# Kernel optimization log

Hardware: AMD Instinct MI355X
Metric: run time of the kernel (lower is better)

## Reference

```python
import jax, jax.numpy as jnp
import numpy as np

B, S, H = 8, 160, 128
W_SIZE, V_SIZE, A_SIZE = 300, 35, 74


def setup_inputs() -> dict:
    key = jax.random.key(0)
    keys = iter(jax.random.split(key, 80))

    def rn(shape, scale=0.05):
        return jax.random.normal(next(keys), shape, dtype=jnp.float32) * scale

    inp = {}
    inp["w"] = rn((B, S, W_SIZE), 1.0)
    inp["v"] = rn((B, S, V_SIZE), 1.0)
    inp["a"] = rn((B, S, A_SIZE), 1.0)
    inp["lengths"] = jnp.full((B,), S, dtype=jnp.int32)  # full-length sequences

    def add_lstm(p, in_size, h_size):
        inp[p + "_Wih"] = rn((4 * h_size, in_size))
        inp[p + "_Whh"] = rn((4 * h_size, h_size))
        inp[p + "_bih"] = rn((4 * h_size,))
        inp[p + "_bhh"] = rn((4 * h_size,))

    add_lstm("w", W_SIZE, H)
    add_lstm("v", V_SIZE, H)
    add_lstm("a", A_SIZE, H)
    add_lstm("c", 3 * H, 3 * H)

    def add_xattn(p, h):
        inp[p + "_W1"] = rn((h, 2 * h))  # Linear(2h, h)
        inp[p + "_b1"] = rn((h,))
        inp[p + "_w2"] = rn((h,))        # Linear(h, 1, bias=False)

    add_xattn("vw", H)
    add_xattn("aw", H)
    add_xattn("sa", 3 * H)

    inp["mp_w"] = rn((H,))
    inp["mp_b"] = rn((1,))
    inp["fc1_W"] = rn((H, 5 * H))
    inp["fc1_b"] = rn((H,))
    inp["fc2_W"] = rn((1, H))
    inp["fc2_b"] = rn((1,))
    return inp


def lstm(x, Wih, Whh, bih, bhh):
    # single-layer batch_first LSTM, PyTorch gate order (i, f, g, o)
    b = x.shape[0]
    h = Whh.shape[1]
    xg = jnp.einsum('bsi,gi->bsg', x, Wih) + bih + bhh  # [B,S,4H]

    def step(carry, xt):
        hp, cp = carry
        g = xt + hp @ Whh.T
        i, f, gg, o = jnp.split(g, 4, axis=-1)
        c = jax.nn.sigmoid(f) * cp + jax.nn.sigmoid(i) * jnp.tanh(gg)
        hn = jax.nn.sigmoid(o) * jnp.tanh(c)
        return (hn, c), hn

    init = (jnp.zeros((b, h), x.dtype), jnp.zeros((b, h), x.dtype))
    _, hs = jax.lax.scan(step, init, jnp.swapaxes(xg, 0, 1))
    return jnp.swapaxes(hs, 0, 1)  # [B,S,H]


def cross_attention(src_hs, tgt_hs, mask, W1, b1, w2):
    # additive (Bahdanau) attention; attn_1(cat([src, tgt])) split into two GEMMs
    h = src_hs.shape[-1]
    s = src_hs @ W1[:, :h].T              # [B,V,Hd]
    t = tgt_hs @ W1[:, h:].T + b1         # [B,W,Hd]
    # [B,W,V,Hd] broadcast-add + tanh, then reduce with w2 -> scores [B,W,V]
    scores = jnp.einsum('bwvd,d->bwv', jnp.tanh(t[:, :, None, :] + s[:, None, :, :]), w2)
    scores = mask * scores                # multiplicative mask (as in original)
    weights = jax.nn.softmax(scores, axis=2)
    out = jnp.einsum('bwv,bvh->bwh', weights, src_hs)
    return out, weights


def soft_attention(reps, w, b):
    weights = jax.nn.softmax(reps @ w + b[0], axis=1)  # [B,S]
    out = jnp.einsum('bs,bsh->bh', weights, reps)
    return out, weights[:, :, None]


def reference(w, v, a, lengths,
              w_Wih, w_Whh, w_bih, w_bhh,
              v_Wih, v_Whh, v_bih, v_bhh,
              a_Wih, a_Whh, a_bih, a_bhh,
              c_Wih, c_Whh, c_bih, c_bhh,
              vw_W1, vw_b1, vw_w2,
              aw_W1, aw_b1, aw_w2,
              sa_W1, sa_b1, sa_w2,
              mp_w, mp_b, fc1_W, fc1_b, fc2_W, fc2_b):
    b, s = w.shape[0], w.shape[1]
    w_hs = lstm(w, w_Wih, w_Whh, w_bih, w_bhh)
    v_hs = lstm(v, v_Wih, v_Whh, v_bih, v_bhh)
    a_hs = lstm(a, a_Wih, a_Whh, a_bih, a_bhh)

    len_mask = (jnp.arange(s)[None, :] < lengths[:, None]).astype(w_hs.dtype)  # [B,S]
    mask3 = jnp.broadcast_to(len_mask[:, None, :], (b, s, s))                  # [B,W,V]

    v_out, v_attn_w = cross_attention(v_hs, w_hs, mask3, vw_W1, vw_b1, vw_w2)
    a_out, a_attn_w = cross_attention(a_hs, w_hs, mask3, aw_W1, aw_b1, aw_w2)

    c_hs = lstm(jnp.concatenate([w_hs, v_out, a_out], axis=2), c_Wih, c_Whh, c_bih, c_bhh)
    c_attn_out, _ = cross_attention(c_hs, c_hs, mask3, sa_W1, sa_b1, sa_w2)
    c_out = c_attn_out[jnp.arange(b), lengths - 1]  # last valid timestep, [B,3H]

    v_comp, v_soft_w = soft_attention(v_hs, mp_w, mp_b)
    a_comp, a_soft_w = soft_attention(a_hs, mp_w, mp_b)

    feat = jnp.concatenate([c_out, v_comp, a_comp], axis=-1)  # [B,5H]
    out = jax.nn.relu(feat @ fc1_W.T + fc1_b) @ fc2_W.T + fc2_b  # dropout = identity (eval)
    return out.reshape(-1), v_attn_w, v_soft_w, a_attn_w, a_soft_w
```

## Files before the change

### kernel.cpp

```cpp
#include <hip/hip_runtime.h>
#include <hip/hip_fp16.h>

typedef unsigned int u32;
typedef unsigned long long u64;

#define B 8
#define S 160
#define H 128
#define H3 384
#define G4 512
#define CG 1536
#define WIN 300
#define VIN 35
#define AIN 74

#define XG_W   0
#define XG_V   (XG_W + B*S*G4)
#define XG_A   (XG_V + B*S*G4)
#define HS_W   (XG_A + B*S*G4)
#define HS_V   (HS_W + B*S*H)
#define HS_A   (HS_V + B*S*H)
#define S_VW   (HS_A + B*S*H)
#define T_VW   (S_VW + B*S*H)
#define S_AW   (T_VW + B*S*H)
#define T_AW   (S_AW + B*S*H)
#define C_X    (T_AW + B*S*H)
#define S_SA   (C_X + B*S*H3)
#define WIHT_W (S_SA + B*S*H3)
#define WIHT_V (WIHT_W + WIN*G4)
#define WIHT_A (WIHT_V + VIN*G4)
#define WIHT_C (WIHT_A + AIN*G4)
#define WHHT_W (WIHT_C + H3*CG)
#define WHHT_V (WHHT_W + H*G4)
#define WHHT_A (WHHT_V + H*G4)
#define SAT_S  (WHHT_A + H*G4)
#define SAT_T  (SAT_S + H3*H3)
#define VW_ST  (SAT_T + H3*H3)
#define VW_TT  (VW_ST + H*H)
#define AW_ST  (VW_TT + H*H)
#define AW_TT  (AW_ST + H*H)
#define BSUM_W (AW_TT + H*H)
#define BSUM_V (BSUM_W + G4)
#define BSUM_A (BSUM_V + G4)
#define BSUM_C (BSUM_A + G4)
#define VCOMP  (BSUM_C + CG)
#define ACOMP  (VCOMP + B*H)
#define C_OUT  (ACOMP + B*H)
#define XGC16  (C_OUT + B*H3)
#define WRES   (XGC16 + B*S*CG/2)
#define CHS16  (WRES + CG*H3/2)
#define H_X    (CHS16 + B*S*H3/2)

#define O_VATT  8
#define O_VSOFT (8 + B*S*S)
#define O_AATT  (O_VSOFT + B*S)
#define O_ASOFT (O_AATT + B*S*S)

#define REP32(M) M(0)M(1)M(2)M(3)M(4)M(5)M(6)M(7)M(8)M(9)M(10)M(11)M(12)M(13)M(14)M(15)M(16)M(17)M(18)M(19)M(20)M(21)M(22)M(23)M(24)M(25)M(26)M(27)M(28)M(29)M(30)M(31)
#define REP48(M) REP32(M) M(32)M(33)M(34)M(35)M(36)M(37)M(38)M(39)M(40)M(41)M(42)M(43)M(44)M(45)M(46)M(47)

__device__ __forceinline__ float sigf(float x){ return 1.f/(1.f+__expf(-x)); }
__device__ __forceinline__ float tanhfast(float x){ float e=__expf(2.f*x); return 1.f - 2.f/(e+1.f); }
__device__ __forceinline__ float wred_sum(float x){
#pragma unroll
  for (int o=32;o;o>>=1) x += __shfl_xor(x,o);
  return x;
}
__device__ __forceinline__ float wred_max(float x){
#pragma unroll
  for (int o=32;o;o>>=1) x = fmaxf(x,__shfl_xor(x,o));
  return x;
}
__device__ __forceinline__ u32 packh2(float lo, float hi){
  __half a=__float2half_rn(lo), b=__float2half_rn(hi);
  return ((u32)__half_as_ushort(b)<<16) | (u32)__half_as_ushort(a);
}

typedef _Float16 h2v __attribute__((ext_vector_type(2)));
#if defined(__has_builtin)
#if __has_builtin(__builtin_amdgcn_fdot2)
#define HAVE_FDOT2 1
#endif
#endif
__device__ __forceinline__ float fdot2f(u32 w, u32 h, float acc){
#ifdef HAVE_FDOT2
  return __builtin_amdgcn_fdot2(__builtin_bit_cast(h2v,w), __builtin_bit_cast(h2v,h), acc, false);
#else
  h2v a=__builtin_bit_cast(h2v,w), b=__builtin_bit_cast(h2v,h);
  return acc + (float)a.x*(float)b.x + (float)a.y*(float)b.y;
#endif
}

#define PREP_TOT (3*G4 + CG + WIN*G4 + VIN*G4 + AIN*G4 + H3*CG + 3*H*G4 + 2*H3*H3 + 4*H*H + CG*H3/2)
__global__ void k0_prep(float* __restrict__ ws, u32* __restrict__ wsu,
    const float* __restrict__ wWih, const float* __restrict__ wWhh, const float* __restrict__ wbih, const float* __restrict__ wbhh,
    const float* __restrict__ vWih, const float* __restrict__ vWhh, const float* __restrict__ vbih, const float* __restrict__ vbhh,
    const float* __restrict__ aWih, const float* __restrict__ aWhh, const float* __restrict__ abih, const float* __restrict__ abhh,
    const float* __restrict__ cWih, const float* __restrict__ cWhh, const float* __restrict__ cbih, const float* __restrict__ cbhh,
    const float* __restrict__ vwW1, const float* __restrict__ awW1, const float* __restrict__ saW1)
{
  int idx = blockIdx.x*256 + threadIdx.x;
  if (idx >= PREP_TOT) return;
  if (idx < G4){ ws[BSUM_W+idx]=wbih[idx]+wbhh[idx]; return; } idx -= G4;
  if (idx < G4){ ws[BSUM_V+idx]=vbih[idx]+vbhh[idx]; return; } idx -= G4;
  if (idx < G4){ ws[BSUM_A+idx]=abih[idx]+abhh[idx]; return; } idx -= G4;
  if (idx < CG){ ws[BSUM_C+idx]=cbih[idx]+cbhh[idx]; return; } idx -= CG;
  if (idx < WIN*G4){ int k=idx/G4,g=idx%G4; ws[WIHT_W+idx]=wWih[g*WIN+k]; return; } idx -= WIN*G4;
  if (idx < VIN*G4){ int k=idx/G4,g=idx%G4; ws[WIHT_V+idx]=vWih[g*VIN+k]; return; } idx -= VIN*G4;
  if (idx < AIN*G4){ int k=idx/G4,g=idx%G4; ws[WIHT_A+idx]=aWih[g*AIN+k]; return; } idx -= AIN*G4;
  if (idx < H3*CG){ int k=idx/CG,g=idx%CG; ws[WIHT_C+idx]=cWih[g*H3+k]; return; } idx -= H3*CG;
  if (idx < H*G4){ int q=idx&3, r=idx>>2, g=r&511, k4=r>>9; ws[WHHT_W+idx]=wWhh[g*H + 4*k4+q]; return; } idx -= H*G4;
  if (idx < H*G4){ int q=idx&3, r=idx>>2, g=r&511, k4=r>>9; ws[WHHT_V+idx]=vWhh[g*H + 4*k4+q]; return; } idx -= H*G4;
  if (idx < H*G4){ int q=idx&3, r=idx>>2, g=r&511, k4=r>>9; ws[WHHT_A+idx]=aWhh[g*H + 4*k4+q]; return; } idx -= H*G4;
  if (idx < H3*H3){ int k=idx/H3,d=idx%H3; ws[SAT_S+idx]=saW1[d*(2*H3)+k]; return; } idx -= H3*H3;
  if (idx < H3*H3){ int k=idx/H3,d=idx%H3; ws[SAT_T+idx]=saW1[d*(2*H3)+H3+k]; return; } idx -= H3*H3;
  if (idx < H*H){ int k=idx/H,d=idx%H; ws[VW_ST+idx]=vwW1[d*(2*H)+k]; return; } idx -= H*H;
  if (idx < H*H){ int k=idx/H,d=idx%H; ws[VW_TT+idx]=vwW1[d*(2*H)+H+k]; return; } idx -= H*H;
  if (idx < H*H){ int k=idx/H,d=idx%H; ws[AW_ST+idx]=awW1[d*(2*H)+k]; return; } idx -= H*H;
  if (idx < H*H){ int k=idx/H,d=idx%H; ws[AW_TT+idx]=awW1[d*(2*H)+H+k]; return; } idx -= H*H;
  {
    int q = idx & 3; int r = idx >> 2;
    int t = r & 255; int r2 = r >> 8;
    int i = r2 % 48; int sl = r2 / 48;
    int j = t >> 6, ul = t & 63;
    int row = j*H3 + sl*64 + ul;
    int k2 = i*4 + q;
    wsu[WRES+idx] = packh2(cWhh[(size_t)row*H3 + 2*k2], cWhh[(size_t)row*H3 + 2*k2 + 1]);
  }
}

__global__ void k1_xg(float* __restrict__ ws,
    const float* __restrict__ xw, const float* __restrict__ xv, const float* __restrict__ xa)
{
  int bid = blockIdx.x;
  int lstm = bid/160; int rem = bid%160; int b = rem/20; int s0 = (rem%20)*8;
  int in_dim; const float* x; const float* wT; const float* bs; float* xg;
  if (lstm==0){ in_dim=WIN; x=xw; wT=ws+WIHT_W; bs=ws+BSUM_W; xg=ws+XG_W; }
  else if (lstm==1){ in_dim=VIN; x=xv; wT=ws+WIHT_V; bs=ws+BSUM_V; xg=ws+XG_V; }
  else { in_dim=AIN; x=xa; wT=ws+WIHT_A; bs=ws+BSUM_A; xg=ws+XG_A; }
  __shared__ float xt[8][WIN];
  int tid = threadIdx.x;
  for (int i=tid; i<8*in_dim; i+=256){ int r=i/in_dim, k=i%in_dim; xt[r][k] = x[((size_t)(b*S+s0+r))*in_dim + k]; }
  __syncthreads();
  float acc0[8], acc1[8];
  float b0 = bs[tid], b1 = bs[tid+256];
#pragma unroll
  for (int r=0;r<8;r++){ acc0[r]=b0; acc1[r]=b1; }
  for (int k=0;k<in_dim;k++){
    float w0 = wT[k*G4 + tid], w1 = wT[k*G4 + 256 + tid];
#pragma unroll
    for (int r=0;r<8;r++){ float xx = xt[r][k]; acc0[r] = fmaf(xx,w0,acc0[r]); acc1[r] = fmaf(xx,w1,acc1[r]); }
  }
#pragma unroll
  for (int r=0;r<8;r++){
    size_t ro = (size_t)(b*S+s0+r)*G4;
    xg[ro + tid] = acc0[r];
    xg[ro + 256 + tid] = acc1[r];
  }
}

__global__ __launch_bounds__(512,1) void k2_lstm(float* __restrict__ ws)
{
  int lstm = blockIdx.x >> 3, b = blockIdx.x & 7;
  const float* xg; const float* whhT; float* hs; float* cx = nullptr;
  if (lstm==0){ xg=ws+XG_W; whhT=ws+WHHT_W; hs=ws+HS_W; cx=ws+C_X; }
  else if (lstm==1){ xg=ws+XG_V; whhT=ws+WHHT_V; hs=ws+HS_V; }
  else { xg=ws+XG_A; whhT=ws+WHHT_A; hs=ws+HS_A; }
  int g = threadIdx.x;
  const float4* wb = ((const float4*)whhT) + g;
#define K2_LD(i) float4 w##i = wb[(i)*512];
  REP32(K2_LD)
  __shared__ __align__(16) float hbuf[H];
  __shared__ float gsum[G4];
  float c_reg = 0.f;
  if (g < H) hbuf[g] = 0.f;
  const float* xgb = xg + (size_t)b*S*G4;
  float* hsb = hs + (size_t)b*S*H;
  float* cxb = cx ? cx + (size_t)b*S*H3 : nullptr;
  float xg_cur = xgb[g];
  __syncthreads();
  const float4* h4p = (const float4*)hbuf;
  for (int t=0;t<S;t++){
    float acc = xg_cur;
    float xg_nxt = (t+1<S) ? xgb[(size_t)(t+1)*G4 + g] : 0.f;
#define K2_FMA(i) { float4 h4 = h4p[i]; acc = fmaf(w##i.x,h4.x,acc); acc = fmaf(w##i.y,h4.y,acc); acc = fmaf(w##i.z,h4.z,acc); acc = fmaf(w##i.w,h4.w,acc); }
    REP32(K2_FMA)
    gsum[g] = acc;
    xg_cur = xg_nxt;
    __syncthreads();
    if (g < H){
      float gi=gsum[g], gf=gsum[H+g], gg=gsum[2*H+g], go=gsum[3*H+g];
      c_reg = sigf(gf)*c_reg + sigf(gi)*tanhfast(gg);
      float h = sigf(go)*tanhfast(c_reg);
      hbuf[g] = h;
      hsb[(size_t)t*H + g] = h;
      if (cxb) cxb[(size_t)t*H3 + g] = h;
    }
    __syncthreads();
  }
}

__global__ void k3a_proj(float* __restrict__ ws, const float* __restrict__ vwb1, const float* __restrict__ awb1)
{
  int bid = blockIdx.x;
  int p = bid/160; int rem = bid%160; int b = rem/20; int s0 = (rem%20)*8;
  const float* src; const float* wT; const float* bias=nullptr; float* dst;
  if (p==0){ src=ws+HS_V; wT=ws+VW_ST; dst=ws+S_VW; }
  else if (p==1){ src=ws+HS_W; wT=ws+VW_TT; bias=vwb1; dst=ws+T_VW; }
  else if (p==2){ src=ws+HS_A; wT=ws+AW_ST; dst=ws+S_AW; }
  else { src=ws+HS_W; wT=ws+AW_TT; bias=awb1; dst=ws+T_AW; }
  __shared__ float xr[8][H];
  int tid = threadIdx.x;
  for (int i=tid;i<8*H;i+=128){ int r=i>>7, k=i&127; xr[r][k] = src[(size_t)(b*S+s0+r)*H + k]; }
  __syncthreads();
  float acc[8];
  float bv = bias ? bias[tid] : 0.f;
#pragma unroll
  for (int r=0;r<8;r++) acc[r]=bv;
  for (int k=0;k<H;k++){
    float wv = wT[k*H + tid];
#pragma unroll
    for (int r=0;r<8;r++) acc[r] = fmaf(xr[r][k], wv, acc[r]);
  }
#pragma unroll
  for (int r=0;r<8;r++) dst[(size_t)(b*S+s0+r)*H + tid] = acc[r];
}

__global__ void k3b_attn(float* __restrict__ ws, float* __restrict__ dout,
    const int* __restrict__ lengths, const float* __restrict__ vww2, const float* __restrict__ aww2)
{
  int wid = threadIdx.x >> 6, lane = threadIdx.x & 63;
  int row = blockIdx.x*4 + wid;
  int A = row / (B*S); int rem = row % (B*S); int b = rem / S; int w = rem % S;
  const float* sp = ws + (A? S_AW : S_VW) + (size_t)(b*S)*H;
  const float* tp = ws + (A? T_AW : T_VW) + (size_t)(b*S + w)*H;
  const float* w2 = A? aww2 : vww2;
  const float* src = ws + (A? HS_A : HS_V) + (size_t)(b*S)*H;
  float* attw = dout + (A? O_AATT : O_VATT) + (size_t)b*S*S + (size_t)w*S;
  int len = lengths[b];
  __shared__ float sc[4][S];
  float2 t2 = ((const float2*)tp)[lane];
  float2 w22 = ((const float2*)w2)[lane];
  for (int v=0; v<S; v++){
    float2 s2 = ((const float2*)(sp + (size_t)v*H))[lane];
    float x0 = tanhfast(t2.x + s2.x), x1 = tanhfast(t2.y + s2.y);
    float p = wred_sum(x0*w22.x + x1*w22.y);
    if (lane==0) sc[wid][v] = p;
  }
  __syncthreads();
  float m0 = (lane      < len)? sc[wid][lane]     : 0.f;
  float m1 = (lane+64   < len)? sc[wid][lane+64]  : 0.f;
  float m2 = (lane<32) ? ((lane+128 < len)? sc[wid][lane+128] : 0.f) : -1e30f;
  float m = wred_max(fmaxf(fmaxf(m0,m1),m2));
  float e0 = __expf(m0-m), e1 = __expf(m1-m), e2 = (lane<32)? __expf(m2-m) : 0.f;
  float inv = 1.f / wred_sum(e0+e1+e2);
  e0*=inv; e1*=inv; e2*=inv;
  sc[wid][lane] = e0; sc[wid][lane+64] = e1; if (lane<32) sc[wid][128+lane] = e2;
  attw[lane] = e0; attw[lane+64] = e1; if (lane<32) attw[128+lane] = e2;
  __syncthreads();
  float2 acc; acc.x=0.f; acc.y=0.f;
  for (int v=0; v<S; v++){
    float wg = sc[wid][v];
    float2 sv = ((const float2*)(src + (size_t)v*H))[lane];
    acc.x = fmaf(wg, sv.x, acc.x); acc.y = fmaf(wg, sv.y, acc.y);
  }
  float* cxr = ws + C_X + (size_t)(b*S + w)*H3 + (A? 2*H : H);
  ((float2*)cxr)[lane] = acc;
}

__global__ void k4_soft(float* __restrict__ ws, float* __restrict__ dout,
    const float* __restrict__ mpw, const float* __restrict__ mpb)
{
  int A = blockIdx.x >> 3, b = blockIdx.x & 7;
  const float* reps = ws + (A? HS_A : HS_V) + (size_t)(b*S)*H;
  float* softw = dout + (A? O_ASOFT : O_VSOFT) + b*S;
  float* comp = ws + (A? ACOMP : VCOMP) + b*H;
  __shared__ float sc[S]; __shared__ float wg[S];
  int wid = threadIdx.x >> 6, lane = threadIdx.x & 63;
  float bb = mpb[0];
  for (int s=wid; s<S; s+=4){
    float2 r2 = ((const float2*)(reps + (size_t)s*H))[lane];
    float2 m2 = ((const float2*)mpw)[lane];
    float p = wred_sum(r2.x*m2.x + r2.y*m2.y);
    if (lane==0) sc[s] = p + bb;
  }
  __syncthreads();
  if (threadIdx.x < 64){
    float m0 = sc[lane], m1 = sc[lane+64], m2 = (lane<32)? sc[lane+128] : -1e30f;
    float m = wred_max(fmaxf(fmaxf(m0,m1),m2));
    float e0=__expf(m0-m), e1=__expf(m1-m), e2=(lane<32)?__expf(m2-m):0.f;
    float inv = 1.f / wred_sum(e0+e1+e2);
    e0*=inv; e1*=inv; e2*=inv;
    wg[lane]=e0; wg[lane+64]=e1; if (lane<32) wg[128+lane]=e2;
    softw[lane]=e0; softw[lane+64]=e1; if (lane<32) softw[128+lane]=e2;
  }
  __syncthreads();
  if (threadIdx.x < H){
    float acc=0.f;
    for (int s=0;s<S;s++) acc = fmaf(wg[s], reps[(size_t)s*H + threadIdx.x], acc);
    comp[threadIdx.x] = acc;
  }
}

__global__ void k5_xgc(float* __restrict__ ws, u32* __restrict__ wsu)
{
  int b = blockIdx.x/40; int s0 = (blockIdx.x%40)*4;
  const float* cxb = ws + C_X + (size_t)(b*S+s0)*H3;
  const float* wT = ws + WIHT_C;
  const float* bs = ws + BSUM_C;
  __half* xgc = (__half*)(wsu + XGC16);
  __shared__ float xr[4][H3];
  int tid = threadIdx.x;
  for (int i=tid;i<4*H3;i+=512){ int r=i/H3, k=i%H3; xr[r][k]=cxb[(size_t)r*H3+k]; }
  __syncthreads();
  float acc[4][3];
  float b0=bs[tid], b1=bs[tid+512], b2=bs[tid+1024];
#pragma unroll
  for (int r=0;r<4;r++){ acc[r][0]=b0; acc[r][1]=b1; acc[r][2]=b2; }
  for (int k=0;k<H3;k++){
    float w0=wT[(size_t)k*CG+tid], w1=wT[(size_t)k*CG+512+tid], w2v=wT[(size_t)k*CG+1024+tid];
#pragma unroll
    for (int r=0;r<4;r++){
      float xx = xr[r][k];
      acc[r][0]=fmaf(xx,w0,acc[r][0]); acc[r][1]=fmaf(xx,w1,acc[r][1]); acc[r][2]=fmaf(xx,w2v,acc[r][2]);
    }
  }
#pragma unroll
  for (int r=0;r<4;r++){
    size_t ro = (size_t)(b*S + s0+r)*CG;
    xgc[ro + tid]        = __float2half_rn(acc[r][0]);
    xgc[ro + 512 + tid]  = __float2half_rn(acc[r][1]);
    xgc[ro + 1024 + tid] = __float2half_rn(acc[r][2]);
  }
}

__global__ __launch_bounds__(256,1) void k6_clstm(float* __restrict__ ws, u32* __restrict__ wsu)
{
  int b = blockIdx.x & 7, sl = blockIdx.x >> 3;
  int tid = threadIdx.x, j = tid>>6, ul = tid&63;
  const __half* xgb = ((const __half*)(wsu + XGC16)) + (size_t)b*S*CG;
  u32* chsb = wsu + CHS16 + (size_t)b*S*(H3/2);
  u64* slots = (u64*)(wsu + H_X);
  const uint4* wb = ((const uint4*)(wsu + WRES)) + (size_t)sl*48*256 + tid;
#define K6_LD(i) uint4 w##i = wb[(i)*256];
  REP48(K6_LD)
  __shared__ __align__(16) u32 h2[H3/2];
  __shared__ float gsum[256];
  float c_reg = 0.f;
  if (tid < H3/2) h2[tid] = 0u;
  int row = j*H3 + sl*64 + ul;
  float xg_cur = __half2float(xgb[row]);
  __syncthreads();
  const uint4* h2q = (const uint4*)h2;
  for (int t=0;t<S;t++){
    float acc = xg_cur;
#define K6_FD(i) { uint4 hh = h2q[i]; acc = fdot2f(w##i.x,hh.x,acc); acc = fdot2f(w##i.y,hh.y,acc); acc = fdot2f(w##i.z,hh.z,acc); acc = fdot2f(w##i.w,hh.w,acc); }
    REP48(K6_FD)
    float xg_nxt = (t+1<S)? __half2float(xgb[(size_t)(t+1)*CG + row]) : 0.f;
    gsum[tid] = acc;
    xg_cur = xg_nxt;
    __syncthreads();
    int par = t & 1;
    u32 target = (u32)(t>>1) + 1u;
    u64* sb = slots + ((size_t)par*8 + b)*192;
    if (tid < 64){
      float gi=gsum[tid], gf=gsum[64+tid], gg=gsum[128+tid], go=gsum[192+tid];
      c_reg = sigf(gf)*c_reg + sigf(gi)*tanhfast(gg);
      float h = sigf(go)*tanhfast(c_reg);
      float h1 = __shfl_down(h, 1);
      if (!(tid & 1)){
        u32 pk = packh2(h, h1);
        int p = sl*32 + (tid>>1);
        h2[p] = pk;
        chsb[(size_t)t*(H3/2) + p] = pk;
        if (t+1 < S)
          __hip_atomic_store(&sb[p], ((u64)target<<32) | (u64)pk,
                             __ATOMIC_RELAXED, __HIP_MEMORY_SCOPE_AGENT);
      }
    } else if (t+1 < S){
      int i = tid - 64;
      if (i < 160){
        int pi = i >> 5;
        int psl = sl + 1 + pi; if (psl >= 6) psl -= 6;
        int p = psl*32 + (i & 31);
        u64 v;
        do { v = __hip_atomic_load(&sb[p], __ATOMIC_RELAXED, __HIP_MEMORY_SCOPE_AGENT); }
        while ((u32)(v>>32) != target);
        h2[p] = (u32)v;
      }
    }
    __syncthreads();
  }
}

__global__ void k7a_sproj(float* __restrict__ ws, u32* __restrict__ wsu)
{
  int b = blockIdx.x/40; int v0 = (blockIdx.x%40)*4;
  const __half* chs = (const __half*)(wsu + CHS16);
  const float* wT = ws + SAT_S;
  __shared__ float xr[4][H3];
  int tid = threadIdx.x;
  for (int i=tid;i<4*H3;i+=384){ int r=i/H3, k=i%H3; xr[r][k] = __half2float(chs[(size_t)(b*S+v0+r)*H3 + k]); }
  __syncthreads();
  float acc[4] = {0.f,0.f,0.f,0.f};
  for (int k=0;k<H3;k++){
    float wv = wT[(size_t)k*H3 + tid];
#pragma unroll
    for (int r=0;r<4;r++) acc[r] = fmaf(xr[r][k], wv, acc[r]);
  }
#pragma unroll
  for (int r=0;r<4;r++) ws[S_SA + (size_t)(b*S+v0+r)*H3 + tid] = acc[r];
}

__global__ void k7b_sa(float* __restrict__ ws, u32* __restrict__ wsu,
    const int* __restrict__ lengths, const float* __restrict__ sab1, const float* __restrict__ saw2)
{
  int b = blockIdx.x;
  int len = lengths[b]; int tr = len-1;
  const __half* chs = (const __half*)(wsu + CHS16);
  __shared__ float tv[H3]; __shared__ float chr[H3]; __shared__ float sc[S]; __shared__ float wg[S];
  int tid = threadIdx.x, wid = tid>>6, lane = tid&63;
  chr[tid] = __half2float(chs[(size_t)(b*S+tr)*H3 + tid]);
  __syncthreads();
  float acc = sab1[tid];
  for (int k=0;k<H3;k++) acc = fmaf(chr[k], ws[SAT_T + (size_t)k*H3 + tid], acc);
  tv[tid] = acc;
  __syncthreads();
  for (int v=wid; v<S; v+=6){
    const float* sr = ws + S_SA + (size_t)(b*S+v)*H3;
    float p = 0.f;
#pragma unroll
    for (int q=0;q<6;q++){
      int d = lane + 64*q;
      p = fmaf(tanhfast(tv[d] + sr[d]), saw2[d], p);
    }
    p = wred_sum(p);
    if (lane==0) sc[v] = p;
  }
  __syncthreads();
  if (tid < 64){
    float m0 = (lane<len)? sc[lane]:0.f;
    float m1 = (lane+64<len)? sc[lane+64]:0.f;
    float m2 = (lane<32)? ((lane+128<len)? sc[lane+128]:0.f) : -1e30f;
    float m = wred_max(fmaxf(fmaxf(m0,m1),m2));
    float e0=__expf(m0-m), e1=__expf(m1-m), e2=(lane<32)?__expf(m2-m):0.f;
    float inv = 1.f / wred_sum(e0+e1+e2);
    wg[lane]=e0*inv; wg[lane+64]=e1*inv; if (lane<32) wg[128+lane]=e2*inv;
  }
  __syncthreads();
  float o = 0.f;
  for (int v=0; v<S; v++) o = fmaf(wg[v], __half2float(chs[(size_t)(b*S+v)*H3 + tid]), o);
  ws[C_OUT + (size_t)b*H3 + tid] = o;
}

__global__ void k8_mlp(float* __restrict__ ws, float* __restrict__ dout,
    const float* __restrict__ fc1W, const float* __restrict__ fc1b,
    const float* __restrict__ fc2W, const float* __restrict__ fc2b)
{
  int b = blockIdx.x, tid = threadIdx.x;
  __shared__ float feat[5*H]; __shared__ float r1[H];
  for (int i=tid;i<5*H;i+=128){
    float val;
    if (i < H3) val = ws[C_OUT + (size_t)b*H3 + i];
    else if (i < H3+H) val = ws[VCOMP + b*H + (i-H3)];
    else val = ws[ACOMP + b*H + (i-H3-H)];
    feat[i] = val;
  }
  __syncthreads();
  float acc = fc1b[tid];
  for (int k=0;k<5*H;k++) acc = fmaf(feat[k], fc1W[(size_t)tid*5*H + k], acc);
  r1[tid] = fmaxf(acc, 0.f) * fc2W[tid];
  __syncthreads();
  if (tid < 64){
    float p = r1[tid] + r1[tid+64];
    p = wred_sum(p);
    if (tid==0) dout[b] = p + fc2b[0];
  }
}

extern "C" void kernel_launch(void* const* d_in, const int* in_sizes, int n_in,
                              void* d_out, int out_size, void* d_ws, size_t ws_size,
                              hipStream_t stream) {
  const float* xw = (const float*)d_in[0];
  const float* xv = (const float*)d_in[1];
  const float* xa = (const float*)d_in[2];
  const int* lengths = (const int*)d_in[3];
  const float* wWih=(const float*)d_in[4], *wWhh=(const float*)d_in[5], *wbih=(const float*)d_in[6], *wbhh=(const float*)d_in[7];
  const float* vWih=(const float*)d_in[8], *vWhh=(const float*)d_in[9], *vbih=(const float*)d_in[10], *vbhh=(const float*)d_in[11];
  const float* aWih=(const float*)d_in[12], *aWhh=(const float*)d_in[13], *abih=(const float*)d_in[14], *abhh=(const float*)d_in[15];
  const float* cWih=(const float*)d_in[16], *cWhh=(const float*)d_in[17], *cbih=(const float*)d_in[18], *cbhh=(const float*)d_in[19];
  const float* vwW1=(const float*)d_in[20], *vwb1=(const float*)d_in[21], *vww2=(const float*)d_in[22];
  const float* awW1=(const float*)d_in[23], *awb1=(const float*)d_in[24], *aww2=(const float*)d_in[25];
  const float* saW1=(const float*)d_in[26], *sab1=(const float*)d_in[27], *saw2=(const float*)d_in[28];
  const float* mpw=(const float*)d_in[29], *mpb=(const float*)d_in[30];
  const float* fc1W=(const float*)d_in[31], *fc1b=(const float*)d_in[32];
  const float* fc2W=(const float*)d_in[33], *fc2b=(const float*)d_in[34];
  float* ws = (float*)d_ws;
  u32* wsu = (u32*)d_ws;
  float* dout = (float*)d_out;

  hipLaunchKernelGGL(k0_prep, dim3((PREP_TOT+255)/256), dim3(256), 0, stream,
      ws, wsu, wWih,wWhh,wbih,wbhh, vWih,vWhh,vbih,vbhh, aWih,aWhh,abih,abhh,
      cWih,cWhh,cbih,cbhh, vwW1, awW1, saW1);
  hipLaunchKernelGGL(k1_xg, dim3(480), dim3(256), 0, stream, ws, xw, xv, xa);
  hipLaunchKernelGGL(k2_lstm, dim3(24), dim3(512), 0, stream, ws);
  hipLaunchKernelGGL(k3a_proj, dim3(640), dim3(128), 0, stream, ws, vwb1, awb1);
  hipLaunchKernelGGL(k3b_attn, dim3(640), dim3(256), 0, stream, ws, dout, lengths, vww2, aww2);
  hipLaunchKernelGGL(k4_soft, dim3(16), dim3(256), 0, stream, ws, dout, mpw, mpb);
  hipLaunchKernelGGL(k5_xgc, dim3(B*40), dim3(512), 0, stream, ws, wsu);
  hipLaunchKernelGGL(k6_clstm, dim3(48), dim3(256), 0, stream, ws, wsu);
  hipLaunchKernelGGL(k7a_sproj, dim3(B*40), dim3(384), 0, stream, ws, wsu);
  hipLaunchKernelGGL(k7b_sa, dim3(B), dim3(384), 0, stream, ws, wsu, lengths, sab1, saw2);
  hipLaunchKernelGGL(k8_mlp, dim3(B), dim3(128), 0, stream, ws, dout, fc1W, fc1b, fc2W, fc2b);
}
```

Before: 958.4 us.

## Split each LSTM cell's gate dot products across 4 lanes with shuffle reduction

Reorganizes the combined LSTM recurrence so each group of 4 threads owns one hidden cell and computes all four gates over a quarter of the K dimension each. Partial sums are combined with xor shuffles, so every thread in the block runs the cell update. This removes the shared-memory gate-sum buffer and the stage where only 64 threads did the nonlinearities. The weight packing in the prep kernel is permuted to match, and the spin-wait polling gains an s_sleep. The extra shuffles and the redundant cell math on each 4-lane group add work, and the sleep may add latency on the critical cross-block handoff.

```diff
diff --git a/kernel.cpp b/kernel.cpp
--- a/kernel.cpp
+++ b/kernel.cpp
@@ -119,13 +119,14 @@
   if (idx < H*H){ int k=idx/H,d=idx%H; ws[AW_ST+idx]=awW1[d*(2*H)+k]; return; } idx -= H*H;
   if (idx < H*H){ int k=idx/H,d=idx%H; ws[AW_TT+idx]=awW1[d*(2*H)+H+k]; return; } idx -= H*H;
   {
-    int q = idx & 3; int r = idx >> 2;
+    int q4 = idx & 3; int r = idx >> 2;
     int t = r & 255; int r2 = r >> 8;
-    int i = r2 % 48; int sl = r2 / 48;
-    int j = t >> 6, ul = t & 63;
-    int row = j*H3 + sl*64 + ul;
-    int k2 = i*4 + q;
-    wsu[WRES+idx] = packh2(cWhh[(size_t)row*H3 + 2*k2], cWhh[(size_t)row*H3 + 2*k2 + 1]);
+    int j = r2 % 48; int sl = r2 / 48;
+    int m = t >> 2, q = t & 3;
+    int gate = j / 12, ii = j % 12;
+    int grow = gate*H3 + sl*64 + m;
+    int k2 = q*48 + ii*4 + q4;
+    wsu[WRES+idx] = packh2(cWhh[(size_t)grow*H3 + 2*k2], cWhh[(size_t)grow*H3 + 2*k2 + 1]);
   }
 }
 
@@ -337,7 +338,7 @@
 __global__ __launch_bounds__(256,1) void k6_clstm(float* __restrict__ ws, u32* __restrict__ wsu)
 {
   int b = blockIdx.x & 7, sl = blockIdx.x >> 3;
-  int tid = threadIdx.x, j = tid>>6, ul = tid&63;
+  int tid = threadIdx.x, m = tid>>2, q = tid&3;
   const __half* xgb = ((const __half*)(wsu + XGC16)) + (size_t)b*S*CG;
   u32* chsb = wsu + CHS16 + (size_t)b*S*(H3/2);
   u64* slots = (u64*)(wsu + H_X);
@@ -345,50 +346,74 @@
 #define K6_LD(i) uint4 w##i = wb[(i)*256];
   REP48(K6_LD)
   __shared__ __align__(16) u32 h2[H3/2];
-  __shared__ float gsum[256];
   float c_reg = 0.f;
   if (tid < H3/2) h2[tid] = 0u;
-  int row = j*H3 + sl*64 + ul;
-  float xg_cur = __half2float(xgb[row]);
-  __syncthreads();
-  const uint4* h2q = (const uint4*)h2;
+  int cell = sl*64 + m;
+  const __half* xga = xgb + cell;
+  float xi = __half2float(xga[0]);
+  float xf = __half2float(xga[H3]);
+  float xg_ = __half2float(xga[2*H3]);
+  float xo = __half2float(xga[3*H3]);
+  __syncthreads();
+  const uint4* h2q = ((const uint4*)h2) + q*12;
   for (int t=0;t<S;t++){
-    float acc = xg_cur;
-#define K6_FD(i) { uint4 hh = h2q[i]; acc = fdot2f(w##i.x,hh.x,acc); acc = fdot2f(w##i.y,hh.y,acc); acc = fdot2f(w##i.z,hh.z,acc); acc = fdot2f(w##i.w,hh.w,acc); }
-    REP48(K6_FD)
-    float xg_nxt = (t+1<S)? __half2float(xgb[(size_t)(t+1)*CG + row]) : 0.f;
-    gsum[tid] = acc;
-    xg_cur = xg_nxt;
+    float ni=0.f,nf=0.f,ng=0.f,no=0.f;
+    if (t+1 < S){
+      const __half* xn = xga + (size_t)(t+1)*CG;
+      ni=__half2float(xn[0]); nf=__half2float(xn[H3]); ng=__half2float(xn[2*H3]); no=__half2float(xn[3*H3]);
+    }
+    float a0=0.f,a1=0.f,a2=0.f,a3=0.f;
+#define K6_I(i, wA,wB,wC,wD) { uint4 hh = h2q[i]; \
+    a0=fdot2f(wA.x,hh.x,a0); a0=fdot2f(wA.y,hh.y,a0); a0=fdot2f(wA.z,hh.z,a0); a0=fdot2f(wA.w,hh.w,a0); \
+    a1=fdot2f(wB.x,hh.x,a1); a1=fdot2f(wB.y,hh.y,a1); a1=fdot2f(wB.z,hh.z,a1); a1=fdot2f(wB.w,hh.w,a1); \
+    a2=fdot2f(wC.x,hh.x,a2); a2=fdot2f(wC.y,hh.y,a2); a2=fdot2f(wC.z,hh.z,a2); a2=fdot2f(wC.w,hh.w,a2); \
+    a3=fdot2f(wD.x,hh.x,a3); a3=fdot2f(wD.y,hh.y,a3); a3=fdot2f(wD.z,hh.z,a3); a3=fdot2f(wD.w,hh.w,a3); }
+    K6_I(0,  w0,  w12, w24, w36)
+    K6_I(1,  w1,  w13, w25, w37)
+    K6_I(2,  w2,  w14, w26, w38)
+    K6_I(3,  w3,  w15, w27, w39)
+    K6_I(4,  w4,  w16, w28, w40)
+    K6_I(5,  w5,  w17, w29, w41)
+    K6_I(6,  w6,  w18, w30, w42)
+    K6_I(7,  w7,  w19, w31, w43)
+    K6_I(8,  w8,  w20, w32, w44)
+    K6_I(9,  w9,  w21, w33, w45)
+    K6_I(10, w10, w22, w34, w46)
+    K6_I(11, w11, w23, w35, w47)
     __syncthreads();
+    a0 += __shfl_xor(a0,1); a0 += __shfl_xor(a0,2);
+    a1 += __shfl_xor(a1,1); a1 += __shfl_xor(a1,2);
+    a2 += __shfl_xor(a2,1); a2 += __shfl_xor(a2,2);
+    a3 += __shfl_xor(a3,1); a3 += __shfl_xor(a3,2);
+    float gi = a0 + xi, gf = a1 + xf, gg = a2 + xg_, go = a3 + xo;
+    c_reg = sigf(gf)*c_reg + sigf(gi)*tanhfast(gg);
+    float h = sigf(go)*tanhfast(c_reg);
     int par = t & 1;
     u32 target = (u32)(t>>1) + 1u;
     u64* sb = slots + ((size_t)par*8 + b)*192;
-    if (tid < 64){
-      float gi=gsum[tid], gf=gsum[64+tid], gg=gsum[128+tid], go=gsum[192+tid];
-      c_reg = sigf(gf)*c_reg + sigf(gi)*tanhfast(gg);
-      float h = sigf(go)*tanhfast(c_reg);
-      float h1 = __shfl_down(h, 1);
-      if (!(tid & 1)){
-        u32 pk = packh2(h, h1);
-        int p = sl*32 + (tid>>1);
-        h2[p] = pk;
-        chsb[(size_t)t*(H3/2) + p] = pk;
-        if (t+1 < S)
-          __hip_atomic_store(&sb[p], ((u64)target<<32) | (u64)pk,
-                             __ATOMIC_RELAXED, __HIP_MEMORY_SCOPE_AGENT);
+    float h1 = __shfl_down(h, 4);
+    if ((tid & 7) == 0){
+      u32 pk = packh2(h, h1);
+      int p = sl*32 + (tid>>3);
+      h2[p] = pk;
+      if (t+1 < S)
+        __hip_atomic_store(&sb[p], ((u64)target<<32) | (u64)pk,
+                           __ATOMIC_RELAXED, __HIP_MEMORY_SCOPE_AGENT);
+      chsb[(size_t)t*(H3/2) + p] = pk;
+    }
+    if (t+1 < S && tid >= 64 && tid < 224){
+      int i = tid - 64;
+      int pi = i >> 5;
+      int psl = sl + 1 + pi; if (psl >= 6) psl -= 6;
+      int p = psl*32 + (i & 31);
+      u64 v = __hip_atomic_load(&sb[p], __ATOMIC_RELAXED, __HIP_MEMORY_SCOPE_AGENT);
+      while ((u32)(v>>32) != target){
+        __builtin_amdgcn_s_sleep(1);
+        v = __hip_atomic_load(&sb[p], __ATOMIC_RELAXED, __HIP_MEMORY_SCOPE_AGENT);
       }
-    } else if (t+1 < S){
-      int i = tid - 64;
-      if (i < 160){
-        int pi = i >> 5;
-        int psl = sl + 1 + pi; if (psl >= 6) psl -= 6;
-        int p = psl*32 + (i & 31);
-        u64 v;
-        do { v = __hip_atomic_load(&sb[p], __ATOMIC_RELAXED, __HIP_MEMORY_SCOPE_AGENT); }
-        while ((u32)(v>>32) != target);
-        h2[p] = (u32)v;
-      }
+      h2[p] = (u32)v;
     }
+    xi=ni; xf=nf; xg_=ng; xo=no;
     __syncthreads();
   }
 }
```

New measurement: 922.4 us. 3.8% less time.
